# Optimization experiments

Measured on AMD Instinct MI355X. Metric: run time of the kernel, lower is better.

Reference implementation:

```python
import jax, jax.numpy as jnp
import numpy as np

B, T, HID = 16, 512, 1024
NH, NKV, D = 8, 4, 128
THETA = 10000.0


def setup_inputs() -> dict:
    key = jax.random.key(0)
    k0, k1, k2, k3, k4 = jax.random.split(key, 5)
    s = 0.02
    return {
        "hidden_states": jax.random.normal(k0, (B, T, HID), dtype=jnp.float32),
        "Wq": s * jax.random.normal(k1, (HID, NH * D), dtype=jnp.float32),
        "Wk": s * jax.random.normal(k2, (HID, NKV * D), dtype=jnp.float32),
        "Wv": s * jax.random.normal(k3, (HID, NKV * D), dtype=jnp.float32),
        "Wo": s * jax.random.normal(k4, (NH * D, HID), dtype=jnp.float32),
    }


def _rotate_half(x):
    x1, x2 = x[..., : x.shape[-1] // 2], x[..., x.shape[-1] // 2:]
    return jnp.concatenate((-x2, x1), axis=-1)


def reference(hidden_states, Wq, Wk, Wv, Wo):
    b, t, _ = hidden_states.shape
    # projections -> [B, H, T, D]
    q = (hidden_states @ Wq).reshape(b, t, NH, D).transpose(0, 2, 1, 3)
    k = (hidden_states @ Wk).reshape(b, t, NKV, D).transpose(0, 2, 1, 3)
    v = (hidden_states @ Wv).reshape(b, t, NKV, D).transpose(0, 2, 1, 3)

    # RoPE: cos/sin [T, D]
    inv_freq = 1.0 / (THETA ** (jnp.arange(0, D, 2, dtype=jnp.float32) / D))
    freqs = jnp.outer(jnp.arange(t, dtype=jnp.float32), inv_freq)
    emb = jnp.concatenate((freqs, freqs), axis=-1)
    cos, sin = jnp.cos(emb), jnp.sin(emb)
    q = q * cos + _rotate_half(q) * sin
    k = k * cos + _rotate_half(k) * sin

    # repeat_interleave KV heads to match query heads (GQA)
    groups = NH // NKV
    k = jnp.repeat(k, groups, axis=1)  # [B, NH, T, D]
    v = jnp.repeat(v, groups, axis=1)

    scale = 1.0 / jnp.sqrt(jnp.float32(D))
    attn = jnp.einsum("bhtd,bhsd->bhts", q, k) * scale  # [B, NH, T, T]
    causal = jnp.triu(jnp.ones((t, t), dtype=bool), k=1)
    attn = jnp.where(causal, -jnp.inf, attn)
    attn = jax.nn.softmax(attn, axis=-1)  # dropout p=0 (eval)

    out = jnp.einsum("bhts,bhsd->bhtd", attn, v)
    out = out.transpose(0, 2, 1, 3).reshape(b, t, NH * D)
    return out @ Wo  # [B, T, HID]
```

## Files before the change

### kernel.cpp

```cpp
#include <hip/hip_runtime.h>
#include <hip/hip_bf16.h>
#include <math.h>

#define Bn 16
#define Tn 512
#define HIDn 1024
#define NHn 8
#define NKVn 4
#define Dn 128

typedef __attribute__((ext_vector_type(8))) short short8;
typedef __attribute__((ext_vector_type(4))) float floatx4;

__device__ __forceinline__ short bf16r(float f) {
  __hip_bfloat16 h = __float2bfloat16(f);
  return *(short*)&h;
}
__device__ __forceinline__ float bf16f(short s) {
  __hip_bfloat16 h = *(__hip_bfloat16*)&s;
  return __bfloat162float(h);
}

__device__ __forceinline__ void g2l16(const short* g, short* l) {
  __builtin_amdgcn_global_load_lds(
      (const __attribute__((address_space(1))) void*)g,
      (__attribute__((address_space(3))) void*)l, 16, 0, 0);
}

__global__ __launch_bounds__(256) void prep_kernel(const float* __restrict__ X,
                                                   const float* __restrict__ Wq,
                                                   const float* __restrict__ Wk,
                                                   const float* __restrict__ Wv,
                                                   const float* __restrict__ Wo,
                                                   short* __restrict__ Xb,
                                                   short* __restrict__ BtQKV,
                                                   short* __restrict__ Wot) {
  __shared__ float tile[32][33];
  int bid = blockIdx.x;
  if (bid < 4096) {
    int i = bid * 256 + threadIdx.x;
    const float4* p = reinterpret_cast<const float4*>(X) + (size_t)i * 2;
    float4 a = p[0], b = p[1];
    short8 o;
    o[0] = bf16r(a.x); o[1] = bf16r(a.y); o[2] = bf16r(a.z); o[3] = bf16r(a.w);
    o[4] = bf16r(b.x); o[5] = bf16r(b.y); o[6] = bf16r(b.z); o[7] = bf16r(b.w);
    reinterpret_cast<short8*>(Xb)[i] = o;
    return;
  }
  int t = bid - 4096;
  const float* in;
  short* out;
  int N;
  if (t < 1024)      { in = Wq; out = BtQKV;               N = 1024; }
  else if (t < 1536) { t -= 1024; in = Wk; out = BtQKV + 1024 * 1024; N = 512; }
  else if (t < 2048) { t -= 1536; in = Wv; out = BtQKV + 1536 * 1024; N = 512; }
  else               { t -= 2048; in = Wo; out = Wot;                N = 1024; }
  int ntx = N >> 5;
  int n0 = (t % ntx) * 32, k0 = (t / ntx) * 32;
  int tx = threadIdx.x & 31, ty = threadIdx.x >> 5;
  for (int i = 0; i < 32; i += 8)
    tile[ty + i][tx] = in[(size_t)(k0 + ty + i) * N + n0 + tx];
  __syncthreads();
  for (int i = 0; i < 32; i += 8)
    out[(size_t)(n0 + ty + i) * 1024 + k0 + tx] = bf16r(tile[tx][ty + i]);
}

__global__ __launch_bounds__(512, 2) void gemm_qkv(const short* __restrict__ A,
                                                   const short* __restrict__ Bt,
                                                   short* __restrict__ Cqkv,
                                                   short* __restrict__ Vt) {
  __shared__ __align__(16) short SH[65536];
  const int tid = threadIdx.x;
  const int wave = tid >> 6, lane = tid & 63;
  const int quad = lane >> 4, l16 = lane & 15;
  const int wr = wave >> 2, wc = wave & 3;
  int fid = blockIdx.y * 8 + blockIdx.x;
  int swz = (fid & 7) * 32 + (fid >> 3);
  const int bx = swz & 7;
  const int m0 = (swz >> 3) << 8, n0 = bx << 8;
  const int nt = 16;

  floatx4 acc[2][2][4][2];
#pragma unroll
  for (int r = 0; r < 2; ++r)
#pragma unroll
    for (int c = 0; c < 2; ++c)
#pragma unroll
      for (int mi = 0; mi < 4; ++mi)
#pragma unroll
        for (int ni = 0; ni < 2; ++ni)
          acc[r][c][mi][ni] = (floatx4){0.f, 0.f, 0.f, 0.f};

  const int srow = tid >> 3;
  const int schunk = (tid & 7) ^ (srow & 7);

#define STAGE(tile_, src_, row0_, ldso_)                                             \
  do {                                                                               \
    int t_ = (tile_);                                                                \
    if (t_ < nt) {                                                                   \
      short* bb_ = SH + ((t_ & 1) << 15) + (ldso_);                                  \
      const short* sp_ =                                                             \
          (src_) + ((size_t)((row0_) + srow) << 10) + (t_ << 6) + (schunk << 3);     \
      g2l16(sp_, bb_ + (wave << 9));                                                 \
      g2l16(sp_ + (64 << 10), bb_ + 4096 + (wave << 9));                             \
    }                                                                                \
  } while (0)

#define LDA(rhalf_)                                                                  \
  do {                                                                               \
    _Pragma("unroll") for (int mi = 0; mi < 4; ++mi) {                               \
      int R = (rhalf_) * 128 + wr * 64 + mi * 16 + l16;                              \
      _Pragma("unroll") for (int k = 0; k < 2; ++k) {                                \
        int pos = (k * 4 + quad) ^ (R & 7);                                          \
        af[mi][k] = *(const short8*)&Ab[R * 64 + pos * 8];                           \
      }                                                                              \
    }                                                                                \
  } while (0)

#define LDB(dst_, chalf_)                                                            \
  do {                                                                               \
    _Pragma("unroll") for (int ni = 0; ni < 2; ++ni) {                               \
      int R = (chalf_) * 128 + wc * 32 + ni * 16 + l16;                              \
      _Pragma("unroll") for (int k = 0; k < 2; ++k) {                                \
        int pos = (k * 4 + quad) ^ (R & 7);                                          \
        dst_[ni][k] = *(const short8*)&Bb[R * 64 + pos * 8];                         \
      }                                                                              \
    }                                                                                \
  } while (0)

#define MFMA_Q(r_, c_, bf_)                                                          \
  do {                                                                               \
    _Pragma("unroll") for (int mi = 0; mi < 4; ++mi)                                 \
        _Pragma("unroll") for (int ni = 0; ni < 2; ++ni) {                           \
      acc[r_][c_][mi][ni] = __builtin_amdgcn_mfma_f32_16x16x32_bf16(                 \
          af[mi][0], bf_[ni][0], acc[r_][c_][mi][ni], 0, 0, 0);                      \
      acc[r_][c_][mi][ni] = __builtin_amdgcn_mfma_f32_16x16x32_bf16(                 \
          af[mi][1], bf_[ni][1], acc[r_][c_][mi][ni], 0, 0, 0);                      \
    }                                                                                \
  } while (0)

#define PH_OPEN()                                                                    \
  do {                                                                               \
    __builtin_amdgcn_s_barrier();                                                    \
    asm volatile("s_waitcnt lgkmcnt(0)");                                            \
    __builtin_amdgcn_s_setprio(1);                                                   \
  } while (0)
#define PH_CLOSE()                                                                   \
  do {                                                                               \
    __builtin_amdgcn_s_setprio(0);                                                   \
    __builtin_amdgcn_s_barrier();                                                    \
  } while (0)

  STAGE(0, A, m0, 0);
  STAGE(0, Bt, n0 + 128, 24576);
  STAGE(0, Bt, n0, 16384);
  STAGE(0, A, m0 + 128, 8192);
  STAGE(1, A, m0, 0);
  STAGE(1, Bt, n0 + 128, 24576);
  STAGE(1, Bt, n0, 16384);
  asm volatile("s_waitcnt vmcnt(6)" ::: "memory");
  __builtin_amdgcn_s_barrier();

  short8 af[4][2], bf0[2][2], bf1[2][2];
  for (int g = 0; g < nt; ++g) {
    const short* Ab = SH + ((g & 1) << 15);
    const short* Bb = Ab + 16384;
    LDA(0);
    LDB(bf0, 0);
    STAGE(g + 1, A, m0 + 128, 8192);
    PH_OPEN();
    MFMA_Q(0, 0, bf0);
    PH_CLOSE();
    LDB(bf1, 1);
    STAGE(g + 2, A, m0, 0);
    PH_OPEN();
    MFMA_Q(0, 1, bf1);
    PH_CLOSE();
    LDA(1);
    STAGE(g + 2, Bt, n0 + 128, 24576);
    PH_OPEN();
    MFMA_Q(1, 1, bf1);
    PH_CLOSE();
    STAGE(g + 2, Bt, n0, 16384);
    PH_OPEN();
    MFMA_Q(1, 0, bf0);
    __builtin_amdgcn_s_setprio(0);
    if (g + 2 < nt)
      asm volatile("s_waitcnt vmcnt(6)" ::: "memory");
    else
      asm volatile("s_waitcnt vmcnt(0)" ::: "memory");
    __builtin_amdgcn_s_barrier();
  }

  if (bx < 6) {
#pragma unroll
    for (int r = 0; r < 2; ++r)
#pragma unroll
      for (int c = 0; c < 2; ++c)
#pragma unroll
        for (int mi = 0; mi < 4; ++mi)
#pragma unroll
          for (int ni = 0; ni < 2; ++ni)
#pragma unroll
            for (int rr = 0; rr < 4; ++rr) {
              int row = m0 + r * 128 + wr * 64 + mi * 16 + quad * 4 + rr;
              int col = n0 + c * 128 + wc * 32 + ni * 16 + l16;
              Cqkv[(size_t)row * 2048 + col] = bf16r(acc[r][c][mi][ni][rr]);
            }
  } else {
    const int b = m0 >> 9, t0 = m0 & (Tn - 1);
#pragma unroll
    for (int ch = 0; ch < 2; ++ch) {
      __syncthreads();
#pragma unroll
      for (int r = 0; r < 2; ++r)
#pragma unroll
        for (int mi = 0; mi < 4; ++mi)
#pragma unroll
          for (int ni = 0; ni < 2; ++ni)
#pragma unroll
            for (int rr = 0; rr < 4; ++rr) {
              int t = r * 128 + wr * 64 + mi * 16 + quad * 4 + rr;
              int d = wc * 32 + ni * 16 + l16;
              SH[d * 264 + t] = bf16r(acc[r][ch][mi][ni][rr]);
            }
      __syncthreads();
      int kv = (bx - 6) * 2 + ch;
#pragma unroll
      for (int u = 0; u < 8; ++u) {
        int idx = tid + u * 512;
        int d = idx >> 5, tb = (idx & 31) << 3;
        short8 vv = *(short8*)&SH[d * 264 + tb];
        *(short8*)&Vt[((size_t)(b * NKVn + kv) * 128 + d) * Tn + t0 + tb] = vv;
      }
    }
  }
#undef STAGE
#undef LDA
#undef LDB
#undef MFMA_Q
#undef PH_OPEN
#undef PH_CLOSE
}

__global__ void rope_k_kernel(short* __restrict__ C) {
  int idx = blockIdx.x * blockDim.x + threadIdx.x;
  int vec = idx & 7;
  int head = (idx >> 3) & 3;
  int bt = idx >> 5;
  int t = bt & (Tn - 1);
  int i0 = vec * 8;
  size_t base = (size_t)bt * 2048 + 1024 + head * 128 + i0;
  short8 x1 = *(short8*)&C[base];
  short8 x2 = *(short8*)&C[base + 64];
  short8 o1, o2;
  float tf = (float)t;
#pragma unroll
  for (int j = 0; j < 8; ++j) {
    float a = tf * exp2f(-0.2076205059f * (float)(i0 + j));
    float s, c;
    sincosf(a, &s, &c);
    float v1 = bf16f(x1[j]), v2 = bf16f(x2[j]);
    o1[j] = bf16r(v1 * c - v2 * s);
    o2[j] = bf16r(v2 * c + v1 * s);
  }
  *(short8*)&C[base] = o1;
  *(short8*)&C[base + 64] = o2;
}

template <bool OUTF32>
__global__ __launch_bounds__(256) void gemm_bt(const short* __restrict__ A,
                                               const short* __restrict__ Bt,
                                               void* __restrict__ Cout,
                                               int M, int N, int K) {
  __shared__ __align__(16) short As[128 * 64];
  __shared__ __align__(16) short Bs[128 * 64];
  const int tid = threadIdx.x;
  const int wave = tid >> 6, lane = tid & 63;
  const int quad = lane >> 4, l16 = lane & 15;
  const int wrow = wave >> 1, wcol = wave & 1;
  const int m0 = blockIdx.y * 128, n0 = blockIdx.x * 128;
  floatx4 acc[4][4];
  for (int mi = 0; mi < 4; ++mi)
    for (int ni = 0; ni < 4; ++ni)
      acc[mi][ni] = (floatx4){0.f, 0.f, 0.f, 0.f};

  for (int kt = 0; kt < K; kt += 64) {
#pragma unroll
    for (int v = 0; v < 4; ++v) {
      int s = tid + v * 256;
      int r = s >> 3;
      int c = (s & 7) ^ (r & 7);
      short* dstA = (short*)As + (size_t)(v * 256 + wave * 64) * 8;
      g2l16(&A[(size_t)(m0 + r) * K + kt + c * 8], dstA);
      short* dstB = (short*)Bs + (size_t)(v * 256 + wave * 64) * 8;
      g2l16(&Bt[(size_t)(n0 + r) * K + kt + c * 8], dstB);
    }
    __syncthreads();
#pragma unroll
    for (int kc = 0; kc < 2; ++kc) {
      short8 af[4], bfr[4];
#pragma unroll
      for (int mi = 0; mi < 4; ++mi) {
        int R = wrow * 64 + mi * 16 + l16;
        int pos = (kc * 4 + quad) ^ (R & 7);
        af[mi] = *(short8*)&As[R * 64 + pos * 8];
      }
#pragma unroll
      for (int ni = 0; ni < 4; ++ni) {
        int R = wcol * 64 + ni * 16 + l16;
        int pos = (kc * 4 + quad) ^ (R & 7);
        bfr[ni] = *(short8*)&Bs[R * 64 + pos * 8];
      }
#pragma unroll
      for (int mi = 0; mi < 4; ++mi)
#pragma unroll
        for (int ni = 0; ni < 4; ++ni)
          acc[mi][ni] = __builtin_amdgcn_mfma_f32_16x16x32_bf16(af[mi], bfr[ni], acc[mi][ni], 0, 0, 0);
    }
    __syncthreads();
  }
#pragma unroll
  for (int mi = 0; mi < 4; ++mi)
#pragma unroll
    for (int ni = 0; ni < 4; ++ni)
#pragma unroll
      for (int r = 0; r < 4; ++r) {
        int row = m0 + wrow * 64 + mi * 16 + quad * 4 + r;
        int col = n0 + wcol * 64 + ni * 16 + l16;
        if (OUTF32)
          ((float*)Cout)[(size_t)row * N + col] = acc[mi][ni][r];
        else
          ((short*)Cout)[(size_t)row * N + col] = bf16r(acc[mi][ni][r]);
      }
}

__global__ __launch_bounds__(256) void attn_kernel(const short* __restrict__ Cqkv,
                                                   const short* __restrict__ Vt,
                                                   short* __restrict__ Aout) {
  __shared__ __align__(16) short Ks[64 * 128];
  __shared__ __align__(16) short Vs[128 * 64];
  __shared__ short Ps[4][16][72];
  const int tid = threadIdx.x;
  const int wave = tid >> 6, lane = tid & 63;
  const int quad = lane >> 4, l16 = lane & 15;
  const int blk = blockIdx.x;
  const int qt = 7 - (blk >> 7);
  const int h = blk & 7, b = (blk >> 3) & 15;
  const int kvh = h >> 1;
  const short* Qp = Cqkv + (size_t)b * Tn * 2048 + h * 128;
  const short* Kp = Cqkv + (size_t)b * Tn * 2048 + 1024 + kvh * 128;
  const short* Vtp = Vt + (size_t)(b * NKVn + kvh) * 128 * Tn;

  const int qrow0 = qt * 64 + wave * 16;
  const float scale = 0.08838834764831845f;

  short8 qf[4];
#pragma unroll
  for (int kc = 0; kc < 4; ++kc)
    qf[kc] = *(const short8*)&Qp[(size_t)(qrow0 + l16) * 2048 + kc * 32 + quad * 8];
  {
    float tf = (float)(qrow0 + l16);
#pragma unroll
    for (int kc = 0; kc < 2; ++kc)
#pragma unroll
      for (int j = 0; j < 8; ++j) {
        int d = kc * 32 + quad * 8 + j;
        float a = tf * exp2f(-0.2076205059f * (float)d);
        float s, c;
        sincosf(a, &s, &c);
        float x1 = bf16f(qf[kc][j]), x2 = bf16f(qf[kc + 2][j]);
        qf[kc][j] = bf16r((x1 * c - x2 * s) * scale);
        qf[kc + 2][j] = bf16r((x2 * c + x1 * s) * scale);
      }
  }

  floatx4 o[8];
  float l_part[4];
#pragma unroll
  for (int ni = 0; ni < 8; ++ni) o[ni] = (floatx4){0.f, 0.f, 0.f, 0.f};
#pragma unroll
  for (int r = 0; r < 4; ++r) l_part[r] = 0.f;

  const int nk = qt * 64 + 64;

  for (int k0 = 0; k0 < nk; k0 += 64) {
#pragma unroll
    for (int v = 0; v < 4; ++v) {
      int s = tid + v * 256;
      int r = s >> 4, c = (s & 15) ^ (r & 15);
      short* dstK = (short*)Ks + (size_t)(v * 256 + wave * 64) * 8;
      g2l16(&Kp[(size_t)(k0 + r) * 2048 + c * 8], dstK);
    }
#pragma unroll
    for (int v = 0; v < 4; ++v) {
      int s = tid + v * 256;
      int r = s >> 3, c = (s & 7) ^ (r & 7);
      short* dstV = (short*)Vs + (size_t)(v * 256 + wave * 64) * 8;
      g2l16(&Vtp[(size_t)r * Tn + k0 + c * 8], dstV);
    }
    __syncthreads();

    floatx4 s[4];
#pragma unroll
    for (int ni = 0; ni < 4; ++ni) {
      s[ni] = (floatx4){0.f, 0.f, 0.f, 0.f};
      short8 kf[4];
#pragma unroll
      for (int kc = 0; kc < 4; ++kc) {
        int R = ni * 16 + l16;
        int pos = (kc * 4 + quad) ^ (R & 15);
        kf[kc] = *(short8*)&Ks[R * 128 + pos * 8];
      }
#pragma unroll
      for (int kc = 0; kc < 4; ++kc)
        s[ni] = __builtin_amdgcn_mfma_f32_16x16x32_bf16(qf[kc], kf[kc], s[ni], 0, 0, 0);
    }

    const bool diag = (k0 + 63 > qrow0);
#pragma unroll
    for (int ni = 0; ni < 4; ++ni)
#pragma unroll
      for (int r = 0; r < 4; ++r) {
        float p = __expf(s[ni][r]);
        if (diag) {
          int key = k0 + ni * 16 + l16;
          int qr = qrow0 + quad * 4 + r;
          if (key > qr) p = 0.f;
        }
        s[ni][r] = p;
        l_part[r] += p;
      }

#pragma unroll
    for (int ni = 0; ni < 4; ++ni)
#pragma unroll
      for (int r = 0; r < 4; ++r)
        Ps[wave][quad * 4 + r][ni * 16 + l16] = bf16r(s[ni][r]);

    short8 pf[2];
#pragma unroll
    for (int kc = 0; kc < 2; ++kc)
      pf[kc] = *(short8*)&Ps[wave][l16][kc * 32 + quad * 8];
#pragma unroll
    for (int ni = 0; ni < 8; ++ni) {
      int R = ni * 16 + l16;
      int pos0 = quad ^ (R & 7);
      int pos1 = (4 + quad) ^ (R & 7);
      short8 vf0 = *(short8*)&Vs[R * 64 + pos0 * 8];
      short8 vf1 = *(short8*)&Vs[R * 64 + pos1 * 8];
      o[ni] = __builtin_amdgcn_mfma_f32_16x16x32_bf16(pf[0], vf0, o[ni], 0, 0, 0);
      o[ni] = __builtin_amdgcn_mfma_f32_16x16x32_bf16(pf[1], vf1, o[ni], 0, 0, 0);
    }
    __syncthreads();
  }

  float inv[4];
#pragma unroll
  for (int r = 0; r < 4; ++r) {
    float rs = l_part[r];
#pragma unroll
    for (int off = 8; off >= 1; off >>= 1) rs += __shfl_xor(rs, off, 16);
    inv[r] = 1.0f / rs;
  }
#pragma unroll
  for (int ni = 0; ni < 8; ++ni)
#pragma unroll
    for (int r = 0; r < 4; ++r) {
      int t = qrow0 + quad * 4 + r;
      int d = ni * 16 + l16;
      Aout[((size_t)b * Tn + t) * 1024 + h * 128 + d] = bf16r(o[ni][r] * inv[r]);
    }
}

extern "C" void kernel_launch(void* const* d_in, const int* in_sizes, int n_in,
                              void* d_out, int out_size, void* d_ws, size_t ws_size,
                              hipStream_t stream) {
  const float* X  = (const float*)d_in[0];
  const float* Wq = (const float*)d_in[1];
  const float* Wk = (const float*)d_in[2];
  const float* Wv = (const float*)d_in[3];
  const float* Wo = (const float*)d_in[4];

  char* ws = (char*)d_ws;
  short* Xb    = (short*)(ws);
  short* BtQKV = (short*)(ws + (16ull << 20));
  short* Wot   = (short*)(ws + (20ull << 20));
  short* Cqkv  = (short*)(ws + (22ull << 20));
  short* Vt    = (short*)(ws + (54ull << 20));
  short* Aout  = (short*)(ws + (62ull << 20));

  prep_kernel<<<7168, 256, 0, stream>>>(X, Wq, Wk, Wv, Wo, Xb, BtQKV, Wot);
  gemm_qkv<<<dim3(8, 32), 512, 0, stream>>>(Xb, BtQKV, Cqkv, Vt);
  rope_k_kernel<<<1024, 256, 0, stream>>>(Cqkv);
  attn_kernel<<<1024, 256, 0, stream>>>(Cqkv, Vt, Aout);
  gemm_bt<true><<<dim3(8, 64), 256, 0, stream>>>(Aout, Wot, d_out, 8192, 1024, 1024);
}
```

Measured before the change: 182.1 us.

## Double-buffer K/V tiles in attention with prefetch, exp2 softmax and MFMA priority

Double-buffers the K and V shared-memory tiles so the next tile's global-to-LDS loads are issued before the current tile is computed. This hides load latency and drops one barrier per iteration. The Q scale now folds in log2(e), so exp2f can replace __expf, and s_setprio raises wave priority around the MFMA blocks. LDS use roughly doubles, to about 73KB per block, which may reduce occupancy. There is also a possible race: the prefetch into the other buffer is issued before this iteration's barrier, so it must not overlap other waves' reads of that buffer.

```diff
diff --git a/kernel.cpp b/kernel.cpp
--- a/kernel.cpp
+++ b/kernel.cpp
@@ -338,9 +338,10 @@
 __global__ __launch_bounds__(256) void attn_kernel(const short* __restrict__ Cqkv,
                                                    const short* __restrict__ Vt,
                                                    short* __restrict__ Aout) {
-  __shared__ __align__(16) short Ks[64 * 128];
-  __shared__ __align__(16) short Vs[128 * 64];
-  __shared__ short Ps[4][16][72];
+  __shared__ __align__(16) short SH[37376];
+  short* Ks = SH;
+  short* Vs = SH + 16384;
+  short (*Ps)[16][72] = reinterpret_cast<short(*)[16][72]>(SH + 32768);
   const int tid = threadIdx.x;
   const int wave = tid >> 6, lane = tid & 63;
   const int quad = lane >> 4, l16 = lane & 15;
@@ -353,12 +354,31 @@
   const short* Vtp = Vt + (size_t)(b * NKVn + kvh) * 128 * Tn;
 
   const int qrow0 = qt * 64 + wave * 16;
-  const float scale = 0.08838834764831845f;
+  const float scale = 0.12753378904f;
+
+#define STAGEKV(k0_, b_)                                                      \
+  do {                                                                        \
+    _Pragma("unroll") for (int v = 0; v < 4; ++v) {                           \
+      int s_ = tid + v * 256;                                                 \
+      int r_ = s_ >> 4, c_ = (s_ & 15) ^ (r_ & 15);                           \
+      g2l16(&Kp[(size_t)((k0_) + r_) * 2048 + c_ * 8],                        \
+            Ks + ((b_) << 13) + (v * 256 + wave * 64) * 8);                   \
+    }                                                                         \
+    _Pragma("unroll") for (int v = 0; v < 4; ++v) {                           \
+      int s_ = tid + v * 256;                                                 \
+      int r_ = s_ >> 3, c_ = (s_ & 7) ^ (r_ & 7);                             \
+      g2l16(&Vtp[(size_t)r_ * Tn + (k0_) + c_ * 8],                           \
+            Vs + ((b_) << 13) + (v * 256 + wave * 64) * 8);                   \
+    }                                                                         \
+  } while (0)
 
   short8 qf[4];
 #pragma unroll
   for (int kc = 0; kc < 4; ++kc)
     qf[kc] = *(const short8*)&Qp[(size_t)(qrow0 + l16) * 2048 + kc * 32 + quad * 8];
+
+  STAGEKV(0, 0);
+
   {
     float tf = (float)(qrow0 + l16);
 #pragma unroll
@@ -382,26 +402,19 @@
 #pragma unroll
   for (int r = 0; r < 4; ++r) l_part[r] = 0.f;
 
-  const int nk = qt * 64 + 64;
-
-  for (int k0 = 0; k0 < nk; k0 += 64) {
-#pragma unroll
-    for (int v = 0; v < 4; ++v) {
-      int s = tid + v * 256;
-      int r = s >> 4, c = (s & 15) ^ (r & 15);
-      short* dstK = (short*)Ks + (size_t)(v * 256 + wave * 64) * 8;
-      g2l16(&Kp[(size_t)(k0 + r) * 2048 + c * 8], dstK);
-    }
-#pragma unroll
-    for (int v = 0; v < 4; ++v) {
-      int s = tid + v * 256;
-      int r = s >> 3, c = (s & 7) ^ (r & 7);
-      short* dstV = (short*)Vs + (size_t)(v * 256 + wave * 64) * 8;
-      g2l16(&Vtp[(size_t)r * Tn + k0 + c * 8], dstV);
-    }
-    __syncthreads();
+  const int ntiles = qt + 1;
+  __syncthreads();
+
+  for (int it = 0; it < ntiles; ++it) {
+    const int k0 = it << 6;
+    const int cb = (it & 1) << 13;
+    const short* Kb = Ks + cb;
+    const short* Vb = Vs + cb;
+
+    if (it + 1 < ntiles) STAGEKV(k0 + 64, (it + 1) & 1);
 
     floatx4 s[4];
+    __builtin_amdgcn_s_setprio(1);
 #pragma unroll
     for (int ni = 0; ni < 4; ++ni) {
       s[ni] = (floatx4){0.f, 0.f, 0.f, 0.f};
@@ -410,19 +423,20 @@
       for (int kc = 0; kc < 4; ++kc) {
         int R = ni * 16 + l16;
         int pos = (kc * 4 + quad) ^ (R & 15);
-        kf[kc] = *(short8*)&Ks[R * 128 + pos * 8];
+        kf[kc] = *(short8*)&Kb[R * 128 + pos * 8];
       }
 #pragma unroll
       for (int kc = 0; kc < 4; ++kc)
         s[ni] = __builtin_amdgcn_mfma_f32_16x16x32_bf16(qf[kc], kf[kc], s[ni], 0, 0, 0);
     }
+    __builtin_amdgcn_s_setprio(0);
 
     const bool diag = (k0 + 63 > qrow0);
 #pragma unroll
     for (int ni = 0; ni < 4; ++ni)
 #pragma unroll
       for (int r = 0; r < 4; ++r) {
-        float p = __expf(s[ni][r]);
+        float p = exp2f(s[ni][r]);
         if (diag) {
           int key = k0 + ni * 16 + l16;
           int qr = qrow0 + quad * 4 + r;
@@ -442,18 +456,22 @@
 #pragma unroll
     for (int kc = 0; kc < 2; ++kc)
       pf[kc] = *(short8*)&Ps[wave][l16][kc * 32 + quad * 8];
+    __builtin_amdgcn_s_setprio(1);
 #pragma unroll
     for (int ni = 0; ni < 8; ++ni) {
       int R = ni * 16 + l16;
       int pos0 = quad ^ (R & 7);
       int pos1 = (4 + quad) ^ (R & 7);
-      short8 vf0 = *(short8*)&Vs[R * 64 + pos0 * 8];
-      short8 vf1 = *(short8*)&Vs[R * 64 + pos1 * 8];
+      short8 vf0 = *(short8*)&Vb[R * 64 + pos0 * 8];
+      short8 vf1 = *(short8*)&Vb[R * 64 + pos1 * 8];
       o[ni] = __builtin_amdgcn_mfma_f32_16x16x32_bf16(pf[0], vf0, o[ni], 0, 0, 0);
       o[ni] = __builtin_amdgcn_mfma_f32_16x16x32_bf16(pf[1], vf1, o[ni], 0, 0, 0);
     }
-    __syncthreads();
-  }
+    __builtin_amdgcn_s_setprio(0);
+
+    if (it + 1 < ntiles) __syncthreads();
+  }
+#undef STAGEKV
 
   float inv[4];
 #pragma unroll
```

Result: slower. 187.7 us (+3.1%).
